# Performance work log

Hardware: AMD Instinct MI355X
Metric: run time of the kernel (lower is better)

## Reference

```python
import jax, jax.numpy as jnp
import numpy as np

B, N, DEG, E, Hd, IT = 512, 81, 20, 16, 96, 4


def sudoku_neighbors():
    # 20 constraint neighbors (row/col/box, excluding self) per cell of a 9x9 grid
    n = 9
    nbrs = []
    for r in range(n):
        for c in range(n):
            s = set()
            for k in range(n):
                s.add(r * n + k)
                s.add(k * n + c)
            br, bc = (r // 3) * 3, (c // 3) * 3
            for dr in range(3):
                for dc in range(3):
                    s.add((br + dr) * n + (bc + dc))
            s.discard(r * n + c)
            nbrs.append(sorted(s))
    return np.asarray(nbrs, dtype=np.int32)  # [81, 20]


def mlp3(x, w1, b1, w2, b2, w3, b3):
    # MLP([in, h, h, out]): ReLU between layers, linear output
    x = jax.nn.relu(x @ w1 + b1)
    x = jax.nn.relu(x @ w2 + b2)
    return x @ w3 + b3


def setup_inputs() -> dict:
    key = jax.random.key(0)
    ks = iter(jax.random.split(key, 64))
    W = lambda shape, s=0.05: jax.random.normal(next(ks), shape, jnp.float32) * s
    inp = {
        'grids': jax.random.randint(next(ks), (B, N), 0, 10),
        'nbr': jnp.asarray(sudoku_neighbors()),
        'iters': IT,
        'c0': jax.random.normal(next(ks), (B * N, Hd), jnp.float32),
        'embed_w': W((10, E), 1.0),
        'in_w1': W((E, Hd)), 'in_b1': jnp.zeros((Hd,)),
        'in_w2': W((Hd, Hd)), 'in_b2': jnp.zeros((Hd,)),
        'in_w3': W((Hd, Hd)), 'in_b3': jnp.zeros((Hd,)),
        'f_w1': W((2 * Hd, Hd)), 'f_b1': jnp.zeros((Hd,)),
        'f_w2': W((Hd, Hd)), 'f_b2': jnp.zeros((Hd,)),
        'f_w3': W((Hd, Hd)), 'f_b3': jnp.zeros((Hd,)),
        'g_w1': W((2 * Hd, Hd)), 'g_b1': jnp.zeros((Hd,)),
        'g_w2': W((Hd, Hd)), 'g_b2': jnp.zeros((Hd,)),
        'g_w3': W((Hd, Hd)), 'g_b3': jnp.zeros((Hd,)),
        'lstm_wih': W((Hd, 4 * Hd)), 'lstm_whh': W((Hd, 4 * Hd)),
        'lstm_bih': jnp.zeros((4 * Hd,)), 'lstm_bhh': jnp.zeros((4 * Hd,)),
        'r_w1': W((Hd, Hd)), 'r_b1': jnp.zeros((Hd,)),
        'r_w2': W((Hd, Hd)), 'r_b2': jnp.zeros((Hd,)),
        'r_w3': W((Hd, E)), 'r_b3': jnp.zeros((E,)),
    }
    return inp


def reference(grids, nbr, iters, c0, embed_w,
              in_w1, in_b1, in_w2, in_b2, in_w3, in_b3,
              f_w1, f_b1, f_w2, f_b2, f_w3, f_b3,
              g_w1, g_b1, g_w2, g_b2, g_w3, g_b3,
              lstm_wih, lstm_whh, lstm_bih, lstm_bhh,
              r_w1, r_b1, r_w2, r_b2, r_w3, r_b3):
    X = mlp3(embed_w[grids], in_w1, in_b1, in_w2, in_b2, in_w3, in_b3)  # [B,N,Hd]
    h0 = jax.lax.stop_gradient(X).reshape(B * N, Hd)  # H = X.clone().detach()
    c = c0  # [B*N, Hd]

    def step(carry, _):
        h, c = carry
        H = h.reshape(B, N, Hd)
        Hn = H[:, nbr]  # gather neighbor states [B,N,DEG,Hd]
        pair = jnp.concatenate(
            [jnp.broadcast_to(H[:, :, None, :], Hn.shape), Hn], axis=-1)  # [B,N,DEG,2Hd]
        M = mlp3(pair, f_w1, f_b1, f_w2, f_b2, f_w3, f_b3).sum(axis=2)  # [B,N,Hd]
        x_in = mlp3(jnp.concatenate([X, M], axis=-1),
                    g_w1, g_b1, g_w2, g_b2, g_w3, g_b3).reshape(B * N, Hd)
        gates = x_in @ lstm_wih + lstm_bih + h @ lstm_whh + lstm_bhh
        i, f, g, o = jnp.split(gates, 4, axis=-1)  # torch gate order i,f,g,o
        c2 = jax.nn.sigmoid(f) * c + jax.nn.sigmoid(i) * jnp.tanh(g)
        h2 = jax.nn.sigmoid(o) * jnp.tanh(c2)
        out = mlp3(h2.reshape(B, N, Hd), r_w1, r_b1, r_w2, r_b2, r_w3, r_b3)
        return (h2, c2), out

    _, outs = jax.lax.scan(step, (h0, c), None, length=iters)
    return outs  # [iters, B, N, E]
```

## Files before the change

kernel.cpp:

```cpp
#include <hip/hip_runtime.h>
#include <math.h>

#define Bsz 512
#define Nc  81
#define Rtot (Bsz*Nc)
#define DEG 20
#define Edim 16
#define HD  96
#define NITER 4

typedef __attribute__((ext_vector_type(8))) __bf16 bf16x8;
typedef __attribute__((ext_vector_type(4))) float f32x4;

__device__ __forceinline__ float sigf(float x){ return 1.0f/(1.0f+__expf(-x)); }
__device__ __forceinline__ float tanh_fast(float x){ return 2.0f/(1.0f+__expf(-2.0f*x)) - 1.0f; }

__device__ __forceinline__ unsigned short f2bf(float f){
    union{float f; unsigned u;} v; v.f=f;
    unsigned r = v.u + 0x7fff + ((v.u>>16)&1);
    return (unsigned short)(r>>16);
}
__device__ __forceinline__ float bf2f(unsigned short s){
    union{unsigned u; float f;} v; v.u=((unsigned)s)<<16; return v.f;
}
__device__ __forceinline__ bf16x8 pack8f(const float* x){
    bf16x8 r;
    #pragma unroll
    for (int j=0;j<8;j++) r[j]=(__bf16)x[j];
    return r;
}
__device__ __forceinline__ bf16x8 ldw(const __bf16* p){ return *(const bf16x8*)p; }

__device__ __forceinline__ int swz(int row, int col){
    return row*96 + ((((col>>2) ^ (row&7))<<2) | (col&3));
}
__device__ __forceinline__ void ldtr8(const float* tp, int row, int c, float* o){
    const int r96 = row*96, rho = row&7;
    const float4 a = *(const float4*)(tp + r96 + ((((c>>2)  ) ^ rho)<<2));
    const float4 b = *(const float4*)(tp + r96 + ((((c>>2)+1) ^ rho)<<2));
    o[0]=a.x;o[1]=a.y;o[2]=a.z;o[3]=a.w;o[4]=b.x;o[5]=b.y;o[6]=b.z;o[7]=b.w;
}
__device__ __forceinline__ bf16x8 packtr8(const float* tp, int row, int c){
    float t[8]; ldtr8(tp,row,c,t); return pack8f(t);
}

#define OFF_FW1T 0
#define OFF_FW2T 18432
#define OFF_FW3T 27648
#define OFF_GW1T 36864
#define OFF_GW2T 55296
#define OFF_GW3T 64512
#define OFF_WIHT 73728
#define OFF_WHHT 110592
#define OFF_RW1T 147456
#define OFF_RW2T 156672
#define OFF_RW3T 165888
#define OFF_IW1T 167424
#define OFF_IW2T 170496
#define OFF_IW3T 179712
#define WT_TOTAL 188928

__global__ __launch_bounds__(256) void k_prep(
    const float* __restrict__ fw1, const float* __restrict__ fw2, const float* __restrict__ fw3,
    const float* __restrict__ gw1, const float* __restrict__ gw2, const float* __restrict__ gw3,
    const float* __restrict__ wih, const float* __restrict__ whh,
    const float* __restrict__ rw1, const float* __restrict__ rw2, const float* __restrict__ rw3,
    const float* __restrict__ iw1, const float* __restrict__ iw2, const float* __restrict__ iw3,
    __bf16* __restrict__ wt)
{
    int i = blockIdx.x*256 + threadIdx.x;
    if (i >= WT_TOTAL) return;
    int j = i;
    if (j < 18432){ int n=j/96, k=j-n*96;
        wt[OFF_FW1T+j] = (__bf16)(n<96 ? fw1[k*96+n] : fw1[(96+k)*96+(n-96)]); return; }
    j -= 18432;
    if (j < 9216){ int n=j/96, k=j-n*96; wt[OFF_FW2T+j]=(__bf16)fw2[k*96+n]; return; }
    j -= 9216;
    if (j < 9216){ int n=j/96, k=j-n*96; wt[OFF_FW3T+j]=(__bf16)fw3[k*96+n]; return; }
    j -= 9216;
    if (j < 18432){ int n=j/192, k=j-n*192; wt[OFF_GW1T+j]=(__bf16)gw1[k*96+n]; return; }
    j -= 18432;
    if (j < 9216){ int n=j/96, k=j-n*96; wt[OFF_GW2T+j]=(__bf16)gw2[k*96+n]; return; }
    j -= 9216;
    if (j < 9216){ int n=j/96, k=j-n*96; wt[OFF_GW3T+j]=(__bf16)gw3[k*96+n]; return; }
    j -= 9216;
    if (j < 36864){ int n=j/96, k=j-n*96; wt[OFF_WIHT+j]=(__bf16)wih[k*384+n]; return; }
    j -= 36864;
    if (j < 36864){ int n=j/96, k=j-n*96; wt[OFF_WHHT+j]=(__bf16)whh[k*384+n]; return; }
    j -= 36864;
    if (j < 9216){ int n=j/96, k=j-n*96; wt[OFF_RW1T+j]=(__bf16)rw1[k*96+n]; return; }
    j -= 9216;
    if (j < 9216){ int n=j/96, k=j-n*96; wt[OFF_RW2T+j]=(__bf16)rw2[k*96+n]; return; }
    j -= 9216;
    if (j < 1536){ int n=j/96, k=j-n*96; wt[OFF_RW3T+j]=(__bf16)rw3[k*16+n]; return; }
    j -= 1536;
    if (j < 3072){ int n=j>>5, k=j&31; wt[OFF_IW1T+j]=(__bf16)iw1[(k&15)*96+n]; return; }
    j -= 3072;
    if (j < 9216){ int n=j/96, k=j-n*96; wt[OFF_IW2T+j]=(__bf16)iw2[k*96+n]; return; }
    j -= 9216;
    { int n=j/96, k=j-n*96; wt[OFF_IW3T+j]=(__bf16)iw3[k*96+n]; }
}

__global__ __launch_bounds__(64) void k_embed2(
    const int* __restrict__ grids, const float* __restrict__ embw,
    const __bf16* __restrict__ wt,
    const float* __restrict__ ib1, const float* __restrict__ ib2, const float* __restrict__ ib3,
    __bf16* __restrict__ X, __bf16* __restrict__ Ag, __bf16* __restrict__ Bmg)
{
    __shared__ float tp[16*96];
    const int lane = threadIdx.x & 63;
    const int row16 = lane&15, kgrp = lane>>4, ko = kgrp*8;
    const int rowA = blockIdx.x*16 + row16;
    const int rowO = blockIdx.x*16 + kgrp*4;

    const __bf16* iw1t = wt + OFF_IW1T;
    const __bf16* iw2t = wt + OFF_IW2T;
    const __bf16* iw3t = wt + OFF_IW3T;
    const __bf16* fw1t = wt + OFF_FW1T;

    const int g = grids[rowA];
    const float* ew = embw + g*Edim + (kgrp&1)*8;
    bf16x8 ef;
    #pragma unroll
    for (int j=0;j<8;j++){
        float e = ew[j];
        if (kgrp < 2) ef[j] = (__bf16)e;
        else          ef[j] = (__bf16)(e - bf2f(f2bf(e)));
    }
    #pragma unroll
    for (int nf=0;nf<6;nf++){
        f32x4 c={0.f,0.f,0.f,0.f};
        c=__builtin_amdgcn_mfma_f32_16x16x32_bf16(ef, ldw(iw1t+(size_t)(nf*16+row16)*32+ko), c,0,0,0);
        float b=ib1[nf*16+row16];
        #pragma unroll
        for (int q=0;q<4;q++) tp[swz(kgrp*4+q, nf*16+row16)]=fmaxf(c[q]+b,0.f);
    }
    __syncthreads();
    bf16x8 ta[3];
    #pragma unroll
    for (int kf=0;kf<3;kf++) ta[kf]=packtr8(tp,row16,kf*32+ko);
    __syncthreads();
    #pragma unroll
    for (int nf=0;nf<6;nf++){
        f32x4 c={0.f,0.f,0.f,0.f};
        #pragma unroll
        for (int kf=0;kf<3;kf++)
            c=__builtin_amdgcn_mfma_f32_16x16x32_bf16(ta[kf], ldw(iw2t+(size_t)(nf*16+row16)*HD+kf*32+ko), c,0,0,0);
        float b=ib2[nf*16+row16];
        #pragma unroll
        for (int q=0;q<4;q++) tp[swz(kgrp*4+q, nf*16+row16)]=fmaxf(c[q]+b,0.f);
    }
    __syncthreads();
    #pragma unroll
    for (int kf=0;kf<3;kf++) ta[kf]=packtr8(tp,row16,kf*32+ko);
    __syncthreads();
    #pragma unroll
    for (int nf=0;nf<6;nf++){
        f32x4 c={0.f,0.f,0.f,0.f};
        #pragma unroll
        for (int kf=0;kf<3;kf++)
            c=__builtin_amdgcn_mfma_f32_16x16x32_bf16(ta[kf], ldw(iw3t+(size_t)(nf*16+row16)*HD+kf*32+ko), c,0,0,0);
        float b=ib3[nf*16+row16];
        #pragma unroll
        for (int q=0;q<4;q++){
            float v=c[q]+b;
            X[(size_t)(rowO+q)*HD + nf*16+row16]=(__bf16)v;
            tp[swz(kgrp*4+q, nf*16+row16)]=v;
        }
    }
    __syncthreads();
    bf16x8 hf[3];
    #pragma unroll
    for (int kf=0;kf<3;kf++) hf[kf]=packtr8(tp,row16,kf*32+ko);
    #pragma unroll
    for (int nf=0;nf<12;nf++){
        f32x4 c={0.f,0.f,0.f,0.f};
        #pragma unroll
        for (int kf=0;kf<3;kf++)
            c=__builtin_amdgcn_mfma_f32_16x16x32_bf16(hf[kf], ldw(fw1t+(size_t)(nf*16+row16)*HD+kf*32+ko), c,0,0,0);
        __bf16* dst = (nf<6)? Ag : Bmg;
        int col = ((nf<6)? nf : nf-6)*16 + row16;
        #pragma unroll
        for (int q=0;q<4;q++) dst[(size_t)(rowO+q)*HD+col]=(__bf16)c[q];
    }
}

__global__ __launch_bounds__(64) void k_edge(
    const __bf16* __restrict__ Ag, const __bf16* __restrict__ Bmg,
    const int* __restrict__ nbr,
    const float* __restrict__ fb1, const __bf16* __restrict__ fw2t,
    const float* __restrict__ fb2, const __bf16* __restrict__ fw3t,
    const float* __restrict__ fb3,
    __bf16* __restrict__ M)
{
    __shared__ float accs[16*96];
    const int lane = threadIdx.x & 63;
    const int row16 = lane&15, kgrp = lane>>4, ko = kgrp*8;
    const int rowA = blockIdx.x*16 + row16;
    const int iI = rowA % Nc;
    const __bf16* BmB = Bmg + (size_t)(rowA - iI)*HD + ko;

    bf16x8 w2f[3][6];
    #pragma unroll
    for (int kf=0; kf<3; kf++)
        #pragma unroll
        for (int nf=0; nf<6; nf++)
            w2f[kf][nf] = ldw(fw2t + (size_t)(nf*16+row16)*HD + kf*32+ko);

    float a[3][8];
    #pragma unroll
    for (int kf=0;kf<3;kf++){
        bf16x8 av = ldw(Ag + (size_t)rowA*HD + kf*32 + ko);
        #pragma unroll
        for (int j=0;j<8;j++) a[kf][j] = (float)av[j] + fb1[kf*32+ko+j];
    }
    float b2c[6], b3c[6];
    #pragma unroll
    for (int nf=0;nf<6;nf++){ b2c[nf]=fb2[nf*16+row16]; b3c[nf]=20.0f*fb3[nf*16+row16]; }

    f32x4 acc[6];
    #pragma unroll
    for (int nf=0;nf<6;nf++) acc[nf]=(f32x4){0.f,0.f,0.f,0.f};

    const int* nrow = nbr + iI*DEG;
    bf16x8 v0,v1,v2;
    {
        const __bf16* Vb = BmB + (size_t)nrow[0]*HD;
        v0=ldw(Vb); v1=ldw(Vb+32); v2=ldw(Vb+64);
    }
    #pragma unroll 2
    for (int d=0; d<DEG; d++){
        bf16x8 n0,n1,n2;
        {
            int dn = (d+1<DEG)? d+1 : 0;
            const __bf16* Vb = BmB + (size_t)nrow[dn]*HD;
            n0=ldw(Vb); n1=ldw(Vb+32); n2=ldw(Vb+64);
        }
        bf16x8 xf[3];
        {
            float t[8];
            #pragma unroll
            for (int jj=0;jj<8;jj++) t[jj]=fmaxf(a[0][jj]+(float)v0[jj],0.f);
            xf[0]=pack8f(t);
            #pragma unroll
            for (int jj=0;jj<8;jj++) t[jj]=fmaxf(a[1][jj]+(float)v1[jj],0.f);
            xf[1]=pack8f(t);
            #pragma unroll
            for (int jj=0;jj<8;jj++) t[jj]=fmaxf(a[2][jj]+(float)v2[jj],0.f);
            xf[2]=pack8f(t);
        }
        f32x4 c[6];
        #pragma unroll
        for (int nf=0;nf<6;nf++) c[nf]=(f32x4){0.f,0.f,0.f,0.f};
        #pragma unroll
        for (int kf=0;kf<3;kf++)
            #pragma unroll
            for (int nf=0;nf<6;nf++)
                c[nf]=__builtin_amdgcn_mfma_f32_16x16x32_bf16(xf[kf],w2f[kf][nf],c[nf],0,0,0);
        #pragma unroll
        for (int nf=0;nf<6;nf++)
            #pragma unroll
            for (int q2=0;q2<4;q2++)
                acc[nf][q2]+=fmaxf(c[nf][q2]+b2c[nf],0.f);
        v0=n0; v1=n1; v2=n2;
    }

    #pragma unroll
    for (int nf=0;nf<6;nf++)
        #pragma unroll
        for (int q2=0;q2<4;q2++)
            accs[swz(kgrp*4+q2, nf*16+row16)]=acc[nf][q2];
    __syncthreads();

    f32x4 c2[6];
    #pragma unroll
    for (int nf=0;nf<6;nf++) c2[nf]=(f32x4){0.f,0.f,0.f,0.f};
    #pragma unroll
    for (int kf=0;kf<3;kf++){
        float h[8]; ldtr8(accs, row16, kf*32+ko, h);
        bf16x8 hif, lof;
        #pragma unroll
        for (int j=0;j<8;j++){
            unsigned short hs=f2bf(h[j]);
            union{unsigned short s; __bf16 b;} u; u.s=hs;
            hif[j]=u.b; lof[j]=(__bf16)(h[j]-bf2f(hs));
        }
        #pragma unroll
        for (int nf=0;nf<6;nf++){
            bf16x8 w3f = ldw(fw3t + (size_t)(nf*16+row16)*HD + kf*32+ko);
            c2[nf]=__builtin_amdgcn_mfma_f32_16x16x32_bf16(hif,w3f,c2[nf],0,0,0);
            c2[nf]=__builtin_amdgcn_mfma_f32_16x16x32_bf16(lof,w3f,c2[nf],0,0,0);
        }
    }
    const int rowOut = blockIdx.x*16 + kgrp*4;
    #pragma unroll
    for (int nf=0;nf<6;nf++)
        #pragma unroll
        for (int q2=0;q2<4;q2++)
            M[(size_t)(rowOut+q2)*HD + nf*16+row16] = (__bf16)(c2[nf][q2]+b3c[nf]);
}

__global__ __launch_bounds__(64) void k_fused(
    const __bf16* __restrict__ Xg, const __bf16* __restrict__ Mg,
    const __bf16* __restrict__ Hin, __bf16* __restrict__ Hout,
    const float* __restrict__ Cin, float* __restrict__ Cout,
    __bf16* __restrict__ Ag, __bf16* __restrict__ Bmg,
    const __bf16* __restrict__ wt,
    const float* __restrict__ gb1, const float* __restrict__ gb2, const float* __restrict__ gb3,
    const float* __restrict__ bih, const float* __restrict__ bhh,
    const float* __restrict__ rb1, const float* __restrict__ rb2, const float* __restrict__ rb3,
    float* __restrict__ out, int it, int wab)
{
    __shared__ float tp[16*96];
    const int lane = threadIdx.x & 63;
    const int row16 = lane&15, kgrp = lane>>4, ko = kgrp*8;
    const int rowA = blockIdx.x*16 + row16;
    const int rowO = blockIdx.x*16 + kgrp*4;

    const __bf16* fw1t = wt + OFF_FW1T;
    const __bf16* gw1t = wt + OFF_GW1T;
    const __bf16* gw2t = wt + OFF_GW2T;
    const __bf16* gw3t = wt + OFF_GW3T;
    const __bf16* wiht = wt + OFF_WIHT;
    const __bf16* whht = wt + OFF_WHHT;
    const __bf16* rw1t = wt + OFF_RW1T;
    const __bf16* rw2t = wt + OFF_RW2T;
    const __bf16* rw3t = wt + OFF_RW3T;

    bf16x8 xm[6];
    #pragma unroll
    for (int kf=0;kf<3;kf++){
        xm[kf]   = ldw(Xg + (size_t)rowA*HD + kf*32+ko);
        xm[3+kf] = ldw(Mg + (size_t)rowA*HD + kf*32+ko);
    }
    #pragma unroll
    for (int nf=0;nf<6;nf++){
        f32x4 c={0.f,0.f,0.f,0.f};
        #pragma unroll
        for (int kf=0;kf<6;kf++)
            c=__builtin_amdgcn_mfma_f32_16x16x32_bf16(xm[kf], ldw(gw1t+(size_t)(nf*16+row16)*192+kf*32+ko), c,0,0,0);
        float b=gb1[nf*16+row16];
        #pragma unroll
        for (int q=0;q<4;q++) tp[swz(kgrp*4+q, nf*16+row16)]=fmaxf(c[q]+b,0.f);
    }
    __syncthreads();
    bf16x8 ta[3];
    #pragma unroll
    for (int kf=0;kf<3;kf++) ta[kf]=packtr8(tp,row16,kf*32+ko);
    __syncthreads();
    #pragma unroll
    for (int nf=0;nf<6;nf++){
        f32x4 c={0.f,0.f,0.f,0.f};
        #pragma unroll
        for (int kf=0;kf<3;kf++)
            c=__builtin_amdgcn_mfma_f32_16x16x32_bf16(ta[kf], ldw(gw2t+(size_t)(nf*16+row16)*HD+kf*32+ko), c,0,0,0);
        float b=gb2[nf*16+row16];
        #pragma unroll
        for (int q=0;q<4;q++) tp[swz(kgrp*4+q, nf*16+row16)]=fmaxf(c[q]+b,0.f);
    }
    __syncthreads();
    #pragma unroll
    for (int kf=0;kf<3;kf++) ta[kf]=packtr8(tp,row16,kf*32+ko);
    __syncthreads();
    #pragma unroll
    for (int nf=0;nf<6;nf++){
        f32x4 c={0.f,0.f,0.f,0.f};
        #pragma unroll
        for (int kf=0;kf<3;kf++)
            c=__builtin_amdgcn_mfma_f32_16x16x32_bf16(ta[kf], ldw(gw3t+(size_t)(nf*16+row16)*HD+kf*32+ko), c,0,0,0);
        float b=gb3[nf*16+row16];
        #pragma unroll
        for (int q=0;q<4;q++) tp[swz(kgrp*4+q, nf*16+row16)]=c[q]+b;
    }
    __syncthreads();
    bf16x8 xf[3];
    #pragma unroll
    for (int kf=0;kf<3;kf++) xf[kf]=packtr8(tp,row16,kf*32+ko);
    __syncthreads();

    bf16x8 hfa[3];
    #pragma unroll
    for (int kf=0;kf<3;kf++) hfa[kf]=ldw(Hin + (size_t)rowA*HD + kf*32+ko);

    #pragma unroll 2
    for (int nf=0;nf<6;nf++){
        const int col = nf*16+row16;
        f32x4 g4[4];
        #pragma unroll
        for (int g=0;g<4;g++) g4[g]=(f32x4){0.f,0.f,0.f,0.f};
        #pragma unroll
        for (int g=0;g<4;g++){
            #pragma unroll
            for (int kf=0;kf<3;kf++){
                const int kk = kf*32+ko;
                g4[g]=__builtin_amdgcn_mfma_f32_16x16x32_bf16(xf[kf],  ldw(wiht+(size_t)(g*96+col)*HD+kk), g4[g],0,0,0);
                g4[g]=__builtin_amdgcn_mfma_f32_16x16x32_bf16(hfa[kf], ldw(whht+(size_t)(g*96+col)*HD+kk), g4[g],0,0,0);
            }
        }
        float bi=bih[    col]+bhh[    col];
        float bf=bih[ 96+col]+bhh[ 96+col];
        float bg=bih[192+col]+bhh[192+col];
        float bo=bih[288+col]+bhh[288+col];
        #pragma unroll
        for (int q=0;q<4;q++){
            size_t idx=(size_t)(rowO+q)*HD+col;
            float cold=Cin[idx];
            float iv=sigf(g4[0][q]+bi), fv=sigf(g4[1][q]+bf);
            float gv=tanh_fast(g4[2][q]+bg), ov=sigf(g4[3][q]+bo);
            float c2v=fv*cold+iv*gv;
            float h2v=ov*tanh_fast(c2v);
            Cout[idx]=c2v; Hout[idx]=(__bf16)h2v;
            tp[swz(kgrp*4+q,col)]=h2v;
        }
    }
    __syncthreads();

    bf16x8 hf[3];
    #pragma unroll
    for (int kf=0;kf<3;kf++) hf[kf]=packtr8(tp,row16,kf*32+ko);
    __syncthreads();

    if (wab){
        #pragma unroll
        for (int nf=0;nf<12;nf++){
            f32x4 c={0.f,0.f,0.f,0.f};
            #pragma unroll
            for (int kf=0;kf<3;kf++)
                c=__builtin_amdgcn_mfma_f32_16x16x32_bf16(hf[kf], ldw(fw1t+(size_t)(nf*16+row16)*HD+kf*32+ko), c,0,0,0);
            __bf16* dst = (nf<6)? Ag : Bmg;
            int col = ((nf<6)? nf : nf-6)*16 + row16;
            #pragma unroll
            for (int q=0;q<4;q++) dst[(size_t)(rowO+q)*HD+col]=(__bf16)c[q];
        }
    }

    #pragma unroll
    for (int nf=0;nf<6;nf++){
        f32x4 c={0.f,0.f,0.f,0.f};
        #pragma unroll
        for (int kf=0;kf<3;kf++)
            c=__builtin_amdgcn_mfma_f32_16x16x32_bf16(hf[kf], ldw(rw1t+(size_t)(nf*16+row16)*HD+kf*32+ko), c,0,0,0);
        float b=rb1[nf*16+row16];
        #pragma unroll
        for (int q=0;q<4;q++) tp[swz(kgrp*4+q, nf*16+row16)]=fmaxf(c[q]+b,0.f);
    }
    __syncthreads();
    #pragma unroll
    for (int kf=0;kf<3;kf++) ta[kf]=packtr8(tp,row16,kf*32+ko);
    __syncthreads();
    #pragma unroll
    for (int nf=0;nf<6;nf++){
        f32x4 c={0.f,0.f,0.f,0.f};
        #pragma unroll
        for (int kf=0;kf<3;kf++)
            c=__builtin_amdgcn_mfma_f32_16x16x32_bf16(ta[kf], ldw(rw2t+(size_t)(nf*16+row16)*HD+kf*32+ko), c,0,0,0);
        float b=rb2[nf*16+row16];
        #pragma unroll
        for (int q=0;q<4;q++) tp[swz(kgrp*4+q, nf*16+row16)]=fmaxf(c[q]+b,0.f);
    }
    __syncthreads();
    #pragma unroll
    for (int kf=0;kf<3;kf++) ta[kf]=packtr8(tp,row16,kf*32+ko);
    {
        f32x4 c={0.f,0.f,0.f,0.f};
        #pragma unroll
        for (int kf=0;kf<3;kf++)
            c=__builtin_amdgcn_mfma_f32_16x16x32_bf16(ta[kf], ldw(rw3t+(size_t)row16*HD+kf*32+ko), c,0,0,0);
        float b=rb3[row16];
        #pragma unroll
        for (int q=0;q<4;q++)
            out[((size_t)it*Rtot + rowO+q)*Edim + row16]=c[q]+b;
    }
}

extern "C" void kernel_launch(void* const* d_in, const int* in_sizes, int n_in,
                              void* d_out, int out_size, void* d_ws, size_t ws_size,
                              hipStream_t stream) {
    const int*   grids  = (const int*)  d_in[0];
    const int*   nbr    = (const int*)  d_in[1];
    const float* c0     = (const float*)d_in[3];
    const float* embw   = (const float*)d_in[4];
    const float* in_w1  = (const float*)d_in[5];
    const float* in_b1  = (const float*)d_in[6];
    const float* in_w2  = (const float*)d_in[7];
    const float* in_b2  = (const float*)d_in[8];
    const float* in_w3  = (const float*)d_in[9];
    const float* in_b3  = (const float*)d_in[10];
    const float* f_w1   = (const float*)d_in[11];
    const float* f_b1   = (const float*)d_in[12];
    const float* f_w2   = (const float*)d_in[13];
    const float* f_b2   = (const float*)d_in[14];
    const float* f_w3   = (const float*)d_in[15];
    const float* f_b3   = (const float*)d_in[16];
    const float* g_w1   = (const float*)d_in[17];
    const float* g_b1   = (const float*)d_in[18];
    const float* g_w2   = (const float*)d_in[19];
    const float* g_b2   = (const float*)d_in[20];
    const float* g_w3   = (const float*)d_in[21];
    const float* g_b3   = (const float*)d_in[22];
    const float* wih    = (const float*)d_in[23];
    const float* whh    = (const float*)d_in[24];
    const float* bih    = (const float*)d_in[25];
    const float* bhh    = (const float*)d_in[26];
    const float* r_w1   = (const float*)d_in[27];
    const float* r_b1   = (const float*)d_in[28];
    const float* r_w2   = (const float*)d_in[29];
    const float* r_b2   = (const float*)d_in[30];
    const float* r_w3   = (const float*)d_in[31];
    const float* r_b3   = (const float*)d_in[32];

    __bf16* Xb = (__bf16*)d_ws;
    __bf16* Hb = Xb + (size_t)Rtot*HD;
    float*  Cw = (float*)(Hb + (size_t)Rtot*HD);
    __bf16* Aa = (__bf16*)(Cw + (size_t)Rtot*HD);
    __bf16* Bm = Aa + (size_t)Rtot*HD;
    __bf16* Mm = Bm + (size_t)Rtot*HD;
    __bf16* wt = Mm + (size_t)Rtot*HD;
    float* out = (float*)d_out;

    const __bf16* fw2t = wt + OFF_FW2T;
    const __bf16* fw3t = wt + OFF_FW3T;

    hipLaunchKernelGGL(k_prep, dim3((WT_TOTAL+255)/256), dim3(256), 0, stream,
        f_w1, f_w2, f_w3, g_w1, g_w2, g_w3, wih, whh, r_w1, r_w2, r_w3,
        in_w1, in_w2, in_w3, wt);

    hipLaunchKernelGGL(k_embed2, dim3(Rtot/16), dim3(64), 0, stream,
        grids, embw, wt, in_b1, in_b2, in_b3, Xb, Aa, Bm);

    for (int it=0; it<NITER; ++it){
        hipLaunchKernelGGL(k_edge, dim3(Rtot/16), dim3(64), 0, stream,
            Aa, Bm, nbr, f_b1, fw2t, f_b2, fw3t, f_b3, Mm);
        hipLaunchKernelGGL(k_fused, dim3(Rtot/16), dim3(64), 0, stream,
            Xb, Mm,
            (it==0)? Xb : Hb, Hb,
            (it==0)? c0 : Cw, Cw,
            Aa, Bm, wt,
            g_b1, g_b2, g_b3, bih, bhh, r_b1, r_b2, r_b3,
            out, it, (it<NITER-1)?1:0);
    }
}
```

Before: 506.0 us.

## Fuse all iterations into one persistent per-puzzle kernel with LDS-resident neighbor states

Replaces the embed, edge and fused-update kernels (nine launches) with a single kernel where each 384-thread block owns one 81-cell puzzle across all four iterations. Neighbor projections (Bm), the padded f_w2 weights and packed neighbor indices live in LDS, and h/c/X stay in registers. This removes global round trips for the intermediate X/H/C/A/B/M buffers and the launch boundaries between steps. In exchange only 512 blocks run, each with large LDS use that limits occupancy, and 15 of the 96 rows per block are padding.

Measured after the change: 1.922 ms. +279.9%, slower.

```diff
diff --git a/kernel.cpp b/kernel.cpp
--- a/kernel.cpp
+++ b/kernel.cpp
@@ -101,375 +101,383 @@
     { int n=j/96, k=j-n*96; wt[OFF_IW3T+j]=(__bf16)iw3[k*96+n]; }
 }
 
-__global__ __launch_bounds__(64) void k_embed2(
-    const int* __restrict__ grids, const float* __restrict__ embw,
-    const __bf16* __restrict__ wt,
+__global__ __launch_bounds__(256) void k_prep2(
+    const float* __restrict__ fw2, __bf16* __restrict__ wp)
+{
+    int i = blockIdx.x*256 + threadIdx.x;
+    if (i >= 96*104) return;
+    int n=i/104, k=i-n*104;
+    wp[i] = (__bf16)((k<96)? fw2[k*96+n] : 0.f);
+}
+
+__global__ __launch_bounds__(384) void k_all(
+    const int* __restrict__ grids, const int* __restrict__ nbr,
+    const float* __restrict__ c0, const float* __restrict__ embw,
+    const __bf16* __restrict__ wt, const __bf16* __restrict__ wp,
     const float* __restrict__ ib1, const float* __restrict__ ib2, const float* __restrict__ ib3,
-    __bf16* __restrict__ X, __bf16* __restrict__ Ag, __bf16* __restrict__ Bmg)
-{
-    __shared__ float tp[16*96];
-    const int lane = threadIdx.x & 63;
-    const int row16 = lane&15, kgrp = lane>>4, ko = kgrp*8;
-    const int rowA = blockIdx.x*16 + row16;
-    const int rowO = blockIdx.x*16 + kgrp*4;
-
-    const __bf16* iw1t = wt + OFF_IW1T;
-    const __bf16* iw2t = wt + OFF_IW2T;
-    const __bf16* iw3t = wt + OFF_IW3T;
-    const __bf16* fw1t = wt + OFF_FW1T;
-
-    const int g = grids[rowA];
-    const float* ew = embw + g*Edim + (kgrp&1)*8;
-    bf16x8 ef;
-    #pragma unroll
-    for (int j=0;j<8;j++){
-        float e = ew[j];
-        if (kgrp < 2) ef[j] = (__bf16)e;
-        else          ef[j] = (__bf16)(e - bf2f(f2bf(e)));
-    }
-    #pragma unroll
-    for (int nf=0;nf<6;nf++){
-        f32x4 c={0.f,0.f,0.f,0.f};
-        c=__builtin_amdgcn_mfma_f32_16x16x32_bf16(ef, ldw(iw1t+(size_t)(nf*16+row16)*32+ko), c,0,0,0);
-        float b=ib1[nf*16+row16];
-        #pragma unroll
-        for (int q=0;q<4;q++) tp[swz(kgrp*4+q, nf*16+row16)]=fmaxf(c[q]+b,0.f);
-    }
-    __syncthreads();
-    bf16x8 ta[3];
-    #pragma unroll
-    for (int kf=0;kf<3;kf++) ta[kf]=packtr8(tp,row16,kf*32+ko);
-    __syncthreads();
-    #pragma unroll
-    for (int nf=0;nf<6;nf++){
-        f32x4 c={0.f,0.f,0.f,0.f};
-        #pragma unroll
-        for (int kf=0;kf<3;kf++)
-            c=__builtin_amdgcn_mfma_f32_16x16x32_bf16(ta[kf], ldw(iw2t+(size_t)(nf*16+row16)*HD+kf*32+ko), c,0,0,0);
-        float b=ib2[nf*16+row16];
-        #pragma unroll
-        for (int q=0;q<4;q++) tp[swz(kgrp*4+q, nf*16+row16)]=fmaxf(c[q]+b,0.f);
-    }
-    __syncthreads();
-    #pragma unroll
-    for (int kf=0;kf<3;kf++) ta[kf]=packtr8(tp,row16,kf*32+ko);
-    __syncthreads();
-    #pragma unroll
-    for (int nf=0;nf<6;nf++){
-        f32x4 c={0.f,0.f,0.f,0.f};
-        #pragma unroll
-        for (int kf=0;kf<3;kf++)
-            c=__builtin_amdgcn_mfma_f32_16x16x32_bf16(ta[kf], ldw(iw3t+(size_t)(nf*16+row16)*HD+kf*32+ko), c,0,0,0);
-        float b=ib3[nf*16+row16];
-        #pragma unroll
-        for (int q=0;q<4;q++){
-            float v=c[q]+b;
-            X[(size_t)(rowO+q)*HD + nf*16+row16]=(__bf16)v;
-            tp[swz(kgrp*4+q, nf*16+row16)]=v;
-        }
-    }
-    __syncthreads();
-    bf16x8 hf[3];
-    #pragma unroll
-    for (int kf=0;kf<3;kf++) hf[kf]=packtr8(tp,row16,kf*32+ko);
-    #pragma unroll
-    for (int nf=0;nf<12;nf++){
-        f32x4 c={0.f,0.f,0.f,0.f};
-        #pragma unroll
-        for (int kf=0;kf<3;kf++)
-            c=__builtin_amdgcn_mfma_f32_16x16x32_bf16(hf[kf], ldw(fw1t+(size_t)(nf*16+row16)*HD+kf*32+ko), c,0,0,0);
-        __bf16* dst = (nf<6)? Ag : Bmg;
-        int col = ((nf<6)? nf : nf-6)*16 + row16;
-        #pragma unroll
-        for (int q=0;q<4;q++) dst[(size_t)(rowO+q)*HD+col]=(__bf16)c[q];
-    }
-}
-
-__global__ __launch_bounds__(64) void k_edge(
-    const __bf16* __restrict__ Ag, const __bf16* __restrict__ Bmg,
-    const int* __restrict__ nbr,
-    const float* __restrict__ fb1, const __bf16* __restrict__ fw2t,
-    const float* __restrict__ fb2, const __bf16* __restrict__ fw3t,
-    const float* __restrict__ fb3,
-    __bf16* __restrict__ M)
-{
-    __shared__ float accs[16*96];
-    const int lane = threadIdx.x & 63;
-    const int row16 = lane&15, kgrp = lane>>4, ko = kgrp*8;
-    const int rowA = blockIdx.x*16 + row16;
-    const int iI = rowA % Nc;
-    const __bf16* BmB = Bmg + (size_t)(rowA - iI)*HD + ko;
-
-    bf16x8 w2f[3][6];
-    #pragma unroll
-    for (int kf=0; kf<3; kf++)
-        #pragma unroll
-        for (int nf=0; nf<6; nf++)
-            w2f[kf][nf] = ldw(fw2t + (size_t)(nf*16+row16)*HD + kf*32+ko);
-
-    float a[3][8];
-    #pragma unroll
-    for (int kf=0;kf<3;kf++){
-        bf16x8 av = ldw(Ag + (size_t)rowA*HD + kf*32 + ko);
-        #pragma unroll
-        for (int j=0;j<8;j++) a[kf][j] = (float)av[j] + fb1[kf*32+ko+j];
-    }
-    float b2c[6], b3c[6];
-    #pragma unroll
-    for (int nf=0;nf<6;nf++){ b2c[nf]=fb2[nf*16+row16]; b3c[nf]=20.0f*fb3[nf*16+row16]; }
-
-    f32x4 acc[6];
-    #pragma unroll
-    for (int nf=0;nf<6;nf++) acc[nf]=(f32x4){0.f,0.f,0.f,0.f};
-
-    const int* nrow = nbr + iI*DEG;
-    bf16x8 v0,v1,v2;
-    {
-        const __bf16* Vb = BmB + (size_t)nrow[0]*HD;
-        v0=ldw(Vb); v1=ldw(Vb+32); v2=ldw(Vb+64);
-    }
-    #pragma unroll 2
-    for (int d=0; d<DEG; d++){
-        bf16x8 n0,n1,n2;
-        {
-            int dn = (d+1<DEG)? d+1 : 0;
-            const __bf16* Vb = BmB + (size_t)nrow[dn]*HD;
-            n0=ldw(Vb); n1=ldw(Vb+32); n2=ldw(Vb+64);
-        }
-        bf16x8 xf[3];
-        {
-            float t[8];
-            #pragma unroll
-            for (int jj=0;jj<8;jj++) t[jj]=fmaxf(a[0][jj]+(float)v0[jj],0.f);
-            xf[0]=pack8f(t);
-            #pragma unroll
-            for (int jj=0;jj<8;jj++) t[jj]=fmaxf(a[1][jj]+(float)v1[jj],0.f);
-            xf[1]=pack8f(t);
-            #pragma unroll
-            for (int jj=0;jj<8;jj++) t[jj]=fmaxf(a[2][jj]+(float)v2[jj],0.f);
-            xf[2]=pack8f(t);
-        }
-        f32x4 c[6];
-        #pragma unroll
-        for (int nf=0;nf<6;nf++) c[nf]=(f32x4){0.f,0.f,0.f,0.f};
-        #pragma unroll
-        for (int kf=0;kf<3;kf++)
-            #pragma unroll
-            for (int nf=0;nf<6;nf++)
-                c[nf]=__builtin_amdgcn_mfma_f32_16x16x32_bf16(xf[kf],w2f[kf][nf],c[nf],0,0,0);
-        #pragma unroll
-        for (int nf=0;nf<6;nf++)
-            #pragma unroll
-            for (int q2=0;q2<4;q2++)
-                acc[nf][q2]+=fmaxf(c[nf][q2]+b2c[nf],0.f);
-        v0=n0; v1=n1; v2=n2;
-    }
-
-    #pragma unroll
-    for (int nf=0;nf<6;nf++)
-        #pragma unroll
-        for (int q2=0;q2<4;q2++)
-            accs[swz(kgrp*4+q2, nf*16+row16)]=acc[nf][q2];
-    __syncthreads();
-
-    f32x4 c2[6];
-    #pragma unroll
-    for (int nf=0;nf<6;nf++) c2[nf]=(f32x4){0.f,0.f,0.f,0.f};
-    #pragma unroll
-    for (int kf=0;kf<3;kf++){
-        float h[8]; ldtr8(accs, row16, kf*32+ko, h);
-        bf16x8 hif, lof;
-        #pragma unroll
-        for (int j=0;j<8;j++){
-            unsigned short hs=f2bf(h[j]);
-            union{unsigned short s; __bf16 b;} u; u.s=hs;
-            hif[j]=u.b; lof[j]=(__bf16)(h[j]-bf2f(hs));
-        }
-        #pragma unroll
-        for (int nf=0;nf<6;nf++){
-            bf16x8 w3f = ldw(fw3t + (size_t)(nf*16+row16)*HD + kf*32+ko);
-            c2[nf]=__builtin_amdgcn_mfma_f32_16x16x32_bf16(hif,w3f,c2[nf],0,0,0);
-            c2[nf]=__builtin_amdgcn_mfma_f32_16x16x32_bf16(lof,w3f,c2[nf],0,0,0);
-        }
-    }
-    const int rowOut = blockIdx.x*16 + kgrp*4;
-    #pragma unroll
-    for (int nf=0;nf<6;nf++)
-        #pragma unroll
-        for (int q2=0;q2<4;q2++)
-            M[(size_t)(rowOut+q2)*HD + nf*16+row16] = (__bf16)(c2[nf][q2]+b3c[nf]);
-}
-
-__global__ __launch_bounds__(64) void k_fused(
-    const __bf16* __restrict__ Xg, const __bf16* __restrict__ Mg,
-    const __bf16* __restrict__ Hin, __bf16* __restrict__ Hout,
-    const float* __restrict__ Cin, float* __restrict__ Cout,
-    __bf16* __restrict__ Ag, __bf16* __restrict__ Bmg,
-    const __bf16* __restrict__ wt,
+    const float* __restrict__ fb1, const float* __restrict__ fb2, const float* __restrict__ fb3,
     const float* __restrict__ gb1, const float* __restrict__ gb2, const float* __restrict__ gb3,
     const float* __restrict__ bih, const float* __restrict__ bhh,
     const float* __restrict__ rb1, const float* __restrict__ rb2, const float* __restrict__ rb3,
-    float* __restrict__ out, int it, int wab)
+    float* __restrict__ out)
 {
-    __shared__ float tp[16*96];
-    const int lane = threadIdx.x & 63;
+    __shared__ __bf16 bmL[96*104];
+    __shared__ __bf16 w2L[96*104];
+    __shared__ float  scr[6*16*96];
+    __shared__ unsigned nbrB[405];
+
+    const int tid = threadIdx.x;
+    const int wave = tid/64, lane = tid&63;
     const int row16 = lane&15, kgrp = lane>>4, ko = kgrp*8;
-    const int rowA = blockIdx.x*16 + row16;
-    const int rowO = blockIdx.x*16 + kgrp*4;
-
-    const __bf16* fw1t = wt + OFF_FW1T;
-    const __bf16* gw1t = wt + OFF_GW1T;
-    const __bf16* gw2t = wt + OFF_GW2T;
-    const __bf16* gw3t = wt + OFF_GW3T;
-    const __bf16* wiht = wt + OFF_WIHT;
-    const __bf16* whht = wt + OFF_WHHT;
-    const __bf16* rw1t = wt + OFF_RW1T;
-    const __bf16* rw2t = wt + OFF_RW2T;
-    const __bf16* rw3t = wt + OFF_RW3T;
-
-    bf16x8 xm[6];
-    #pragma unroll
-    for (int kf=0;kf<3;kf++){
-        xm[kf]   = ldw(Xg + (size_t)rowA*HD + kf*32+ko);
-        xm[3+kf] = ldw(Mg + (size_t)rowA*HD + kf*32+ko);
+    const int p = blockIdx.x;
+    const int cellR = wave*16 + row16;
+    const int gcell = (cellR < Nc) ? cellR : Nc-1;
+    float* tp = scr + wave*(16*96);
+
+    const __bf16 *iw1t=wt+OFF_IW1T, *iw2t=wt+OFF_IW2T, *iw3t=wt+OFF_IW3T;
+    const __bf16 *fw1t=wt+OFF_FW1T, *fw3t=wt+OFF_FW3T;
+    const __bf16 *gw1t=wt+OFF_GW1T, *gw2t=wt+OFF_GW2T, *gw3t=wt+OFF_GW3T;
+    const __bf16 *wiht=wt+OFF_WIHT, *whht=wt+OFF_WHHT;
+    const __bf16 *rw1t=wt+OFF_RW1T, *rw2t=wt+OFF_RW2T, *rw3t=wt+OFF_RW3T;
+
+    {
+        const int4* s=(const int4*)wp; int4* d=(int4*)w2L;
+        for (int i=tid;i<(96*104/8);i+=384) d[i]=s[i];
+    }
+    for (int i=tid;i<405;i+=384){
+        unsigned b0=(unsigned)nbr[4*i], b1=(unsigned)nbr[4*i+1],
+                 b2=(unsigned)nbr[4*i+2], b3=(unsigned)nbr[4*i+3];
+        nbrB[i] = b0 | (b1<<8) | (b2<<16) | (b3<<24);
+    }
+
+    float  cC[6][4];
+    bf16x8 xF[3], hF[3];
+    bf16x8 aBb[3];
+
+    {
+        const int g = grids[p*Nc + gcell];
+        const float* ew = embw + g*Edim + (kgrp&1)*8;
+        bf16x8 ef;
+        #pragma unroll
+        for (int j=0;j<8;j++){
+            float e = ew[j];
+            ef[j] = (kgrp<2) ? (__bf16)e : (__bf16)(e - bf2f(f2bf(e)));
+        }
+        #pragma unroll
+        for (int nf=0;nf<6;nf++){
+            f32x4 c={0.f,0.f,0.f,0.f};
+            c=__builtin_amdgcn_mfma_f32_16x16x32_bf16(ef, ldw(iw1t+(size_t)(nf*16+row16)*32+ko), c,0,0,0);
+            float b=ib1[nf*16+row16];
+            #pragma unroll
+            for (int q=0;q<4;q++) tp[swz(kgrp*4+q,nf*16+row16)]=fmaxf(c[q]+b,0.f);
+        }
+        bf16x8 ta[3];
+        #pragma unroll
+        for (int kf=0;kf<3;kf++) ta[kf]=packtr8(tp,row16,kf*32+ko);
+        #pragma unroll
+        for (int nf=0;nf<6;nf++){
+            f32x4 c={0.f,0.f,0.f,0.f};
+            #pragma unroll
+            for (int kf=0;kf<3;kf++)
+                c=__builtin_amdgcn_mfma_f32_16x16x32_bf16(ta[kf], ldw(iw2t+(size_t)(nf*16+row16)*HD+kf*32+ko), c,0,0,0);
+            float b=ib2[nf*16+row16];
+            #pragma unroll
+            for (int q=0;q<4;q++) tp[swz(kgrp*4+q,nf*16+row16)]=fmaxf(c[q]+b,0.f);
+        }
+        #pragma unroll
+        for (int kf=0;kf<3;kf++) ta[kf]=packtr8(tp,row16,kf*32+ko);
+        #pragma unroll
+        for (int nf=0;nf<6;nf++){
+            f32x4 c={0.f,0.f,0.f,0.f};
+            #pragma unroll
+            for (int kf=0;kf<3;kf++)
+                c=__builtin_amdgcn_mfma_f32_16x16x32_bf16(ta[kf], ldw(iw3t+(size_t)(nf*16+row16)*HD+kf*32+ko), c,0,0,0);
+            float b=ib3[nf*16+row16];
+            #pragma unroll
+            for (int q=0;q<4;q++) tp[swz(kgrp*4+q,nf*16+row16)]=c[q]+b;
+        }
+        #pragma unroll
+        for (int kf=0;kf<3;kf++){ xF[kf]=packtr8(tp,row16,kf*32+ko); hF[kf]=xF[kf]; }
     }
     #pragma unroll
-    for (int nf=0;nf<6;nf++){
-        f32x4 c={0.f,0.f,0.f,0.f};
-        #pragma unroll
-        for (int kf=0;kf<6;kf++)
-            c=__builtin_amdgcn_mfma_f32_16x16x32_bf16(xm[kf], ldw(gw1t+(size_t)(nf*16+row16)*192+kf*32+ko), c,0,0,0);
-        float b=gb1[nf*16+row16];
-        #pragma unroll
-        for (int q=0;q<4;q++) tp[swz(kgrp*4+q, nf*16+row16)]=fmaxf(c[q]+b,0.f);
+    for (int nf=0;nf<6;nf++)
+        #pragma unroll
+        for (int q=0;q<4;q++){
+            int cell = wave*16 + kgrp*4 + q;
+            cC[nf][q] = (cell<Nc) ? c0[((size_t)p*Nc+cell)*HD + nf*16+row16] : 0.f;
+        }
+    {
+        #pragma unroll
+        for (int nf=0;nf<6;nf++){
+            f32x4 c={0.f,0.f,0.f,0.f};
+            #pragma unroll
+            for (int kf=0;kf<3;kf++)
+                c=__builtin_amdgcn_mfma_f32_16x16x32_bf16(hF[kf], ldw(fw1t+(size_t)(nf*16+row16)*HD+kf*32+ko), c,0,0,0);
+            #pragma unroll
+            for (int q=0;q<4;q++) tp[swz(kgrp*4+q,nf*16+row16)]=c[q];
+        }
+        #pragma unroll
+        for (int kf=0;kf<3;kf++){
+            float h[8]; ldtr8(tp,row16,kf*32+ko,h);
+            #pragma unroll
+            for (int j=0;j<8;j++) h[j]+=fb1[kf*32+ko+j];
+            aBb[kf]=pack8f(h);
+        }
+        #pragma unroll
+        for (int nf=6;nf<12;nf++){
+            f32x4 c={0.f,0.f,0.f,0.f};
+            #pragma unroll
+            for (int kf=0;kf<3;kf++)
+                c=__builtin_amdgcn_mfma_f32_16x16x32_bf16(hF[kf], ldw(fw1t+(size_t)(nf*16+row16)*HD+kf*32+ko), c,0,0,0);
+            int col=(nf-6)*16+row16;
+            #pragma unroll
+            for (int q=0;q<4;q++) bmL[(wave*16+kgrp*4+q)*104 + col]=(__bf16)c[q];
+        }
     }
     __syncthreads();
-    bf16x8 ta[3];
-    #pragma unroll
-    for (int kf=0;kf<3;kf++) ta[kf]=packtr8(tp,row16,kf*32+ko);
-    __syncthreads();
-    #pragma unroll
-    for (int nf=0;nf<6;nf++){
-        f32x4 c={0.f,0.f,0.f,0.f};
-        #pragma unroll
-        for (int kf=0;kf<3;kf++)
-            c=__builtin_amdgcn_mfma_f32_16x16x32_bf16(ta[kf], ldw(gw2t+(size_t)(nf*16+row16)*HD+kf*32+ko), c,0,0,0);
-        float b=gb2[nf*16+row16];
-        #pragma unroll
-        for (int q=0;q<4;q++) tp[swz(kgrp*4+q, nf*16+row16)]=fmaxf(c[q]+b,0.f);
-    }
-    __syncthreads();
-    #pragma unroll
-    for (int kf=0;kf<3;kf++) ta[kf]=packtr8(tp,row16,kf*32+ko);
-    __syncthreads();
-    #pragma unroll
-    for (int nf=0;nf<6;nf++){
-        f32x4 c={0.f,0.f,0.f,0.f};
-        #pragma unroll
-        for (int kf=0;kf<3;kf++)
-            c=__builtin_amdgcn_mfma_f32_16x16x32_bf16(ta[kf], ldw(gw3t+(size_t)(nf*16+row16)*HD+kf*32+ko), c,0,0,0);
-        float b=gb3[nf*16+row16];
-        #pragma unroll
-        for (int q=0;q<4;q++) tp[swz(kgrp*4+q, nf*16+row16)]=c[q]+b;
-    }
-    __syncthreads();
-    bf16x8 xf[3];
-    #pragma unroll
-    for (int kf=0;kf<3;kf++) xf[kf]=packtr8(tp,row16,kf*32+ko);
-    __syncthreads();
-
-    bf16x8 hfa[3];
-    #pragma unroll
-    for (int kf=0;kf<3;kf++) hfa[kf]=ldw(Hin + (size_t)rowA*HD + kf*32+ko);
-
-    #pragma unroll 2
-    for (int nf=0;nf<6;nf++){
-        const int col = nf*16+row16;
-        f32x4 g4[4];
-        #pragma unroll
-        for (int g=0;g<4;g++) g4[g]=(f32x4){0.f,0.f,0.f,0.f};
-        #pragma unroll
-        for (int g=0;g<4;g++){
+
+    for (int it=0; it<NITER; ++it){
+        bf16x8 mF[3];
+        {
+            float b2c[6], b3c[6];
+            #pragma unroll
+            for (int nf=0;nf<6;nf++){ b2c[nf]=fb2[nf*16+row16]; b3c[nf]=20.0f*fb3[nf*16+row16]; }
+            f32x4 acc[6];
+            #pragma unroll
+            for (int nf=0;nf<6;nf++) acc[nf]=(f32x4){0.f,0.f,0.f,0.f};
+            const unsigned char* nbp = (const unsigned char*)nbrB;
+            #pragma unroll 4
+            for (int d=0; d<DEG; d++){
+                int j = nbp[gcell*DEG + d];
+                const __bf16* vb = bmL + j*104 + ko;
+                bf16x8 xf[3];
+                #pragma unroll
+                for (int kf=0;kf<3;kf++){
+                    bf16x8 v = ldw(vb + kf*32);
+                    float t[8];
+                    #pragma unroll
+                    for (int jj=0;jj<8;jj++) t[jj]=fmaxf((float)aBb[kf][jj] + (float)v[jj], 0.f);
+                    xf[kf]=pack8f(t);
+                }
+                f32x4 c[6];
+                #pragma unroll
+                for (int nf=0;nf<6;nf++) c[nf]=(f32x4){0.f,0.f,0.f,0.f};
+                #pragma unroll
+                for (int kf=0;kf<3;kf++)
+                    #pragma unroll
+                    for (int nf=0;nf<6;nf++)
+                        c[nf]=__builtin_amdgcn_mfma_f32_16x16x32_bf16(xf[kf], ldw(w2L+(size_t)(nf*16+row16)*104+kf*32+ko), c[nf],0,0,0);
+                #pragma unroll
+                for (int nf=0;nf<6;nf++)
+                    #pragma unroll
+                    for (int q=0;q<4;q++)
+                        acc[nf][q]+=fmaxf(c[nf][q]+b2c[nf],0.f);
+            }
+            #pragma unroll
+            for (int nf=0;nf<6;nf++)
+                #pragma unroll
+                for (int q=0;q<4;q++) tp[swz(kgrp*4+q,nf*16+row16)]=acc[nf][q];
+            f32x4 c2[6];
+            #pragma unroll
+            for (int nf=0;nf<6;nf++) c2[nf]=(f32x4){0.f,0.f,0.f,0.f};
             #pragma unroll
             for (int kf=0;kf<3;kf++){
-                const int kk = kf*32+ko;
-                g4[g]=__builtin_amdgcn_mfma_f32_16x16x32_bf16(xf[kf],  ldw(wiht+(size_t)(g*96+col)*HD+kk), g4[g],0,0,0);
-                g4[g]=__builtin_amdgcn_mfma_f32_16x16x32_bf16(hfa[kf], ldw(whht+(size_t)(g*96+col)*HD+kk), g4[g],0,0,0);
-            }
-        }
-        float bi=bih[    col]+bhh[    col];
-        float bf=bih[ 96+col]+bhh[ 96+col];
-        float bg=bih[192+col]+bhh[192+col];
-        float bo=bih[288+col]+bhh[288+col];
-        #pragma unroll
-        for (int q=0;q<4;q++){
-            size_t idx=(size_t)(rowO+q)*HD+col;
-            float cold=Cin[idx];
-            float iv=sigf(g4[0][q]+bi), fv=sigf(g4[1][q]+bf);
-            float gv=tanh_fast(g4[2][q]+bg), ov=sigf(g4[3][q]+bo);
-            float c2v=fv*cold+iv*gv;
-            float h2v=ov*tanh_fast(c2v);
-            Cout[idx]=c2v; Hout[idx]=(__bf16)h2v;
-            tp[swz(kgrp*4+q,col)]=h2v;
-        }
-    }
-    __syncthreads();
-
-    bf16x8 hf[3];
-    #pragma unroll
-    for (int kf=0;kf<3;kf++) hf[kf]=packtr8(tp,row16,kf*32+ko);
-    __syncthreads();
-
-    if (wab){
-        #pragma unroll
-        for (int nf=0;nf<12;nf++){
+                float h[8]; ldtr8(tp,row16,kf*32+ko,h);
+                bf16x8 hif, lof;
+                #pragma unroll
+                for (int j=0;j<8;j++){
+                    unsigned short hs=f2bf(h[j]);
+                    union{unsigned short s; __bf16 b;} u; u.s=hs;
+                    hif[j]=u.b; lof[j]=(__bf16)(h[j]-bf2f(hs));
+                }
+                #pragma unroll
+                for (int nf=0;nf<6;nf++){
+                    bf16x8 w3f = ldw(fw3t + (size_t)(nf*16+row16)*HD + kf*32+ko);
+                    c2[nf]=__builtin_amdgcn_mfma_f32_16x16x32_bf16(hif,w3f,c2[nf],0,0,0);
+                    c2[nf]=__builtin_amdgcn_mfma_f32_16x16x32_bf16(lof,w3f,c2[nf],0,0,0);
+                }
+            }
+            #pragma unroll
+            for (int nf=0;nf<6;nf++)
+                #pragma unroll
+                for (int q=0;q<4;q++) tp[swz(kgrp*4+q,nf*16+row16)]=c2[nf][q]+b3c[nf];
+            #pragma unroll
+            for (int kf=0;kf<3;kf++) mF[kf]=packtr8(tp,row16,kf*32+ko);
+        }
+        __syncthreads();
+
+        bf16x8 xinF[3];
+        {
+            #pragma unroll
+            for (int nf=0;nf<6;nf++){
+                f32x4 c={0.f,0.f,0.f,0.f};
+                #pragma unroll
+                for (int kf=0;kf<3;kf++){
+                    c=__builtin_amdgcn_mfma_f32_16x16x32_bf16(xF[kf], ldw(gw1t+(size_t)(nf*16+row16)*192+kf*32+ko), c,0,0,0);
+                    c=__builtin_amdgcn_mfma_f32_16x16x32_bf16(mF[kf], ldw(gw1t+(size_t)(nf*16+row16)*192+96+kf*32+ko), c,0,0,0);
+                }
+                float b=gb1[nf*16+row16];
+                #pragma unroll
+                for (int q=0;q<4;q++) tp[swz(kgrp*4+q,nf*16+row16)]=fmaxf(c[q]+b,0.f);
+            }
+            bf16x8 ta[3];
+            #pragma unroll
+            for (int kf=0;kf<3;kf++) ta[kf]=packtr8(tp,row16,kf*32+ko);
+            #pragma unroll
+            for (int nf=0;nf<6;nf++){
+                f32x4 c={0.f,0.f,0.f,0.f};
+                #pragma unroll
+                for (int kf=0;kf<3;kf++)
+                    c=__builtin_amdgcn_mfma_f32_16x16x32_bf16(ta[kf], ldw(gw2t+(size_t)(nf*16+row16)*HD+kf*32+ko), c,0,0,0);
+                float b=gb2[nf*16+row16];
+                #pragma unroll
+                for (int q=0;q<4;q++) tp[swz(kgrp*4+q,nf*16+row16)]=fmaxf(c[q]+b,0.f);
+            }
+            #pragma unroll
+            for (int kf=0;kf<3;kf++) ta[kf]=packtr8(tp,row16,kf*32+ko);
+            #pragma unroll
+            for (int nf=0;nf<6;nf++){
+                f32x4 c={0.f,0.f,0.f,0.f};
+                #pragma unroll
+                for (int kf=0;kf<3;kf++)
+                    c=__builtin_amdgcn_mfma_f32_16x16x32_bf16(ta[kf], ldw(gw3t+(size_t)(nf*16+row16)*HD+kf*32+ko), c,0,0,0);
+                float b=gb3[nf*16+row16];
+                #pragma unroll
+                for (int q=0;q<4;q++) tp[swz(kgrp*4+q,nf*16+row16)]=c[q]+b;
+            }
+            #pragma unroll
+            for (int kf=0;kf<3;kf++) xinF[kf]=packtr8(tp,row16,kf*32+ko);
+        }
+
+        {
+            float st[6][4];
+            #pragma unroll
+            for (int nf=0;nf<6;nf++){
+                const int row = nf*16+row16;
+                f32x4 c={0.f,0.f,0.f,0.f};
+                #pragma unroll
+                for (int kf=0;kf<3;kf++){
+                    c=__builtin_amdgcn_mfma_f32_16x16x32_bf16(xinF[kf], ldw(wiht+(size_t)row*HD+kf*32+ko), c,0,0,0);
+                    c=__builtin_amdgcn_mfma_f32_16x16x32_bf16(hF[kf],   ldw(whht+(size_t)row*HD+kf*32+ko), c,0,0,0);
+                }
+                float b=bih[row]+bhh[row];
+                #pragma unroll
+                for (int q=0;q<4;q++) st[nf][q]=sigf(c[q]+b);
+            }
+            #pragma unroll
+            for (int nf=0;nf<6;nf++){
+                const int row = 192+nf*16+row16;
+                f32x4 c={0.f,0.f,0.f,0.f};
+                #pragma unroll
+                for (int kf=0;kf<3;kf++){
+                    c=__builtin_amdgcn_mfma_f32_16x16x32_bf16(xinF[kf], ldw(wiht+(size_t)row*HD+kf*32+ko), c,0,0,0);
+                    c=__builtin_amdgcn_mfma_f32_16x16x32_bf16(hF[kf],   ldw(whht+(size_t)row*HD+kf*32+ko), c,0,0,0);
+                }
+                float b=bih[row]+bhh[row];
+                #pragma unroll
+                for (int q=0;q<4;q++) st[nf][q]*=tanh_fast(c[q]+b);
+            }
+            #pragma unroll
+            for (int nf=0;nf<6;nf++){
+                const int row = 96+nf*16+row16;
+                f32x4 c={0.f,0.f,0.f,0.f};
+                #pragma unroll
+                for (int kf=0;kf<3;kf++){
+                    c=__builtin_amdgcn_mfma_f32_16x16x32_bf16(xinF[kf], ldw(wiht+(size_t)row*HD+kf*32+ko), c,0,0,0);
+                    c=__builtin_amdgcn_mfma_f32_16x16x32_bf16(hF[kf],   ldw(whht+(size_t)row*HD+kf*32+ko), c,0,0,0);
+                }
+                float b=bih[row]+bhh[row];
+                #pragma unroll
+                for (int q=0;q<4;q++) cC[nf][q]=sigf(c[q]+b)*cC[nf][q]+st[nf][q];
+            }
+            #pragma unroll
+            for (int nf=0;nf<6;nf++){
+                const int row = 288+nf*16+row16;
+                f32x4 c={0.f,0.f,0.f,0.f};
+                #pragma unroll
+                for (int kf=0;kf<3;kf++){
+                    c=__builtin_amdgcn_mfma_f32_16x16x32_bf16(xinF[kf], ldw(wiht+(size_t)row*HD+kf*32+ko), c,0,0,0);
+                    c=__builtin_amdgcn_mfma_f32_16x16x32_bf16(hF[kf],   ldw(whht+(size_t)row*HD+kf*32+ko), c,0,0,0);
+                }
+                float b=bih[row]+bhh[row];
+                #pragma unroll
+                for (int q=0;q<4;q++){
+                    float h2v = sigf(c[q]+b)*tanh_fast(cC[nf][q]);
+                    tp[swz(kgrp*4+q, nf*16+row16)]=h2v;
+                }
+            }
+            #pragma unroll
+            for (int kf=0;kf<3;kf++) hF[kf]=packtr8(tp,row16,kf*32+ko);
+        }
+
+        if (it < NITER-1){
+            #pragma unroll
+            for (int nf=0;nf<6;nf++){
+                f32x4 c={0.f,0.f,0.f,0.f};
+                #pragma unroll
+                for (int kf=0;kf<3;kf++)
+                    c=__builtin_amdgcn_mfma_f32_16x16x32_bf16(hF[kf], ldw(fw1t+(size_t)(nf*16+row16)*HD+kf*32+ko), c,0,0,0);
+                #pragma unroll
+                for (int q=0;q<4;q++) tp[swz(kgrp*4+q,nf*16+row16)]=c[q];
+            }
+            #pragma unroll
+            for (int kf=0;kf<3;kf++){
+                float h[8]; ldtr8(tp,row16,kf*32+ko,h);
+                #pragma unroll
+                for (int j=0;j<8;j++) h[j]+=fb1[kf*32+ko+j];
+                aBb[kf]=pack8f(h);
+            }
+            #pragma unroll
+            for (int nf=6;nf<12;nf++){
+                f32x4 c={0.f,0.f,0.f,0.f};
+                #pragma unroll
+                for (int kf=0;kf<3;kf++)
+                    c=__builtin_amdgcn_mfma_f32_16x16x32_bf16(hF[kf], ldw(fw1t+(size_t)(nf*16+row16)*HD+kf*32+ko), c,0,0,0);
+                int col=(nf-6)*16+row16;
+                #pragma unroll
+                for (int q=0;q<4;q++) bmL[(wave*16+kgrp*4+q)*104 + col]=(__bf16)c[q];
+            }
+        }
+
+        {
+            #pragma unroll
+            for (int nf=0;nf<6;nf++){
+                f32x4 c={0.f,0.f,0.f,0.f};
+                #pragma unroll
+                for (int kf=0;kf<3;kf++)
+                    c=__builtin_amdgcn_mfma_f32_16x16x32_bf16(hF[kf], ldw(rw1t+(size_t)(nf*16+row16)*HD+kf*32+ko), c,0,0,0);
+                float b=rb1[nf*16+row16];
+                #pragma unroll
+                for (int q=0;q<4;q++) tp[swz(kgrp*4+q,nf*16+row16)]=fmaxf(c[q]+b,0.f);
+            }
+            bf16x8 ta[3];
+            #pragma unroll
+            for (int kf=0;kf<3;kf++) ta[kf]=packtr8(tp,row16,kf*32+ko);
+            #pragma unroll
+            for (int nf=0;nf<6;nf++){
+                f32x4 c={0.f,0.f,0.f,0.f};
+                #pragma unroll
+                for (int kf=0;kf<3;kf++)
+                    c=__builtin_amdgcn_mfma_f32_16x16x32_bf16(ta[kf], ldw(rw2t+(size_t)(nf*16+row16)*HD+kf*32+ko), c,0,0,0);
+                float b=rb2[nf*16+row16];
+                #pragma unroll
+                for (int q=0;q<4;q++) tp[swz(kgrp*4+q,nf*16+row16)]=fmaxf(c[q]+b,0.f);
+            }
+            #pragma unroll
+            for (int kf=0;kf<3;kf++) ta[kf]=packtr8(tp,row16,kf*32+ko);
             f32x4 c={0.f,0.f,0.f,0.f};
             #pragma unroll
             for (int kf=0;kf<3;kf++)
-                c=__builtin_amdgcn_mfma_f32_16x16x32_bf16(hf[kf], ldw(fw1t+(size_t)(nf*16+row16)*HD+kf*32+ko), c,0,0,0);
-            __bf16* dst = (nf<6)? Ag : Bmg;
-            int col = ((nf<6)? nf : nf-6)*16 + row16;
-            #pragma unroll
-            for (int q=0;q<4;q++) dst[(size_t)(rowO+q)*HD+col]=(__bf16)c[q];
-        }
-    }
-
-    #pragma unroll
-    for (int nf=0;nf<6;nf++){
-        f32x4 c={0.f,0.f,0.f,0.f};
-        #pragma unroll
-        for (int kf=0;kf<3;kf++)
-            c=__builtin_amdgcn_mfma_f32_16x16x32_bf16(hf[kf], ldw(rw1t+(size_t)(nf*16+row16)*HD+kf*32+ko), c,0,0,0);
-        float b=rb1[nf*16+row16];
-        #pragma unroll
-        for (int q=0;q<4;q++) tp[swz(kgrp*4+q, nf*16+row16)]=fmaxf(c[q]+b,0.f);
-    }
-    __syncthreads();
-    #pragma unroll
-    for (int kf=0;kf<3;kf++) ta[kf]=packtr8(tp,row16,kf*32+ko);
-    __syncthreads();
-    #pragma unroll
-    for (int nf=0;nf<6;nf++){
-        f32x4 c={0.f,0.f,0.f,0.f};
-        #pragma unroll
-        for (int kf=0;kf<3;kf++)
-            c=__builtin_amdgcn_mfma_f32_16x16x32_bf16(ta[kf], ldw(rw2t+(size_t)(nf*16+row16)*HD+kf*32+ko), c,0,0,0);
-        float b=rb2[nf*16+row16];
-        #pragma unroll
-        for (int q=0;q<4;q++) tp[swz(kgrp*4+q, nf*16+row16)]=fmaxf(c[q]+b,0.f);
-    }
-    __syncthreads();
-    #pragma unroll
-    for (int kf=0;kf<3;kf++) ta[kf]=packtr8(tp,row16,kf*32+ko);
-    {
-        f32x4 c={0.f,0.f,0.f,0.f};
-        #pragma unroll
-        for (int kf=0;kf<3;kf++)
-            c=__builtin_amdgcn_mfma_f32_16x16x32_bf16(ta[kf], ldw(rw3t+(size_t)row16*HD+kf*32+ko), c,0,0,0);
-        float b=rb3[row16];
-        #pragma unroll
-        for (int q=0;q<4;q++)
-            out[((size_t)it*Rtot + rowO+q)*Edim + row16]=c[q]+b;
+                c=__builtin_amdgcn_mfma_f32_16x16x32_bf16(ta[kf], ldw(rw3t+(size_t)row16*HD+kf*32+ko), c,0,0,0);
+            float b=rb3[row16];
+            #pragma unroll
+            for (int q=0;q<4;q++){
+                int cell = wave*16 + kgrp*4 + q;
+                if (cell < Nc)
+                    out[((size_t)it*Rtot + (size_t)p*Nc + cell)*Edim + row16] = c[q]+b;
+            }
+        }
+        __syncthreads();
     }
 }
 
@@ -509,34 +517,22 @@
     const float* r_w3   = (const float*)d_in[31];
     const float* r_b3   = (const float*)d_in[32];
 
-    __bf16* Xb = (__bf16*)d_ws;
-    __bf16* Hb = Xb + (size_t)Rtot*HD;
-    float*  Cw = (float*)(Hb + (size_t)Rtot*HD);
-    __bf16* Aa = (__bf16*)(Cw + (size_t)Rtot*HD);
-    __bf16* Bm = Aa + (size_t)Rtot*HD;
-    __bf16* Mm = Bm + (size_t)Rtot*HD;
-    __bf16* wt = Mm + (size_t)Rtot*HD;
+    __bf16* wt = (__bf16*)d_ws;
+    __bf16* wp = wt + WT_TOTAL;
     float* out = (float*)d_out;
-
-    const __bf16* fw2t = wt + OFF_FW2T;
-    const __bf16* fw3t = wt + OFF_FW3T;
 
     hipLaunchKernelGGL(k_prep, dim3((WT_TOTAL+255)/256), dim3(256), 0, stream,
         f_w1, f_w2, f_w3, g_w1, g_w2, g_w3, wih, whh, r_w1, r_w2, r_w3,
         in_w1, in_w2, in_w3, wt);
-
-    hipLaunchKernelGGL(k_embed2, dim3(Rtot/16), dim3(64), 0, stream,
-        grids, embw, wt, in_b1, in_b2, in_b3, Xb, Aa, Bm);
-
-    for (int it=0; it<NITER; ++it){
-        hipLaunchKernelGGL(k_edge, dim3(Rtot/16), dim3(64), 0, stream,
-            Aa, Bm, nbr, f_b1, fw2t, f_b2, fw3t, f_b3, Mm);
-        hipLaunchKernelGGL(k_fused, dim3(Rtot/16), dim3(64), 0, stream,
-            Xb, Mm,
-            (it==0)? Xb : Hb, Hb,
-            (it==0)? c0 : Cw, Cw,
-            Aa, Bm, wt,
-            g_b1, g_b2, g_b3, bih, bhh, r_b1, r_b2, r_b3,
-            out, it, (it<NITER-1)?1:0);
-    }
-}
+    hipLaunchKernelGGL(k_prep2, dim3((96*104+255)/256), dim3(256), 0, stream,
+        f_w2, wp);
+
+    hipLaunchKernelGGL(k_all, dim3(Bsz), dim3(384), 0, stream,
+        grids, nbr, c0, embw, wt, wp,
+        in_b1, in_b2, in_b3,
+        f_b1, f_b2, f_b3,
+        g_b1, g_b2, g_b3,
+        bih, bhh,
+        r_b1, r_b2, r_b3,
+        out);
+}
```
